# Optimization experiments

Hardware: AMD Instinct MI355X
Metric: run time of the kernel (lower is better)

Reference implementation:

```python
import jax, jax.numpy as jnp
import numpy as np

B, C_IN, H, W = 64, 2048, 14, 14
D, FF, G, NC, NH = 768, 2048, 100, 9605, 8
DF = int(NC / G + 0.999)  # 97
HD = D // NH
EPS = 1e-5


def _ln(x, g, b):
    m = jnp.mean(x, axis=-1, keepdims=True)
    v = jnp.mean(jnp.square(x - m), axis=-1, keepdims=True)
    return (x - m) * jax.lax.rsqrt(v + EPS) * g + b


def setup_inputs() -> dict:
    key = jax.random.key(0)
    ks = jax.random.split(key, 16)
    def xav(k, shape):
        fan_in, fan_out = shape[-1], shape[-2] if len(shape) > 1 else shape[-1]
        std = float(np.sqrt(2.0 / (fan_in + fan_out)))
        return jax.random.normal(k, shape, jnp.float32) * std
    return {
        "x": jax.random.normal(ks[0], (B, C_IN, H, W), jnp.float32),
        "w_embed": xav(ks[1], (D, C_IN)), "b_embed": jnp.zeros((D,), jnp.float32),
        "query_embed": jax.random.normal(ks[2], (G, D), jnp.float32),
        "wq": xav(ks[3], (D, D)), "bq": jnp.zeros((D,), jnp.float32),
        "wk": xav(ks[4], (D, D)), "bk": jnp.zeros((D,), jnp.float32),
        "wv": xav(ks[5], (D, D)), "bv": jnp.zeros((D,), jnp.float32),
        "wo": xav(ks[6], (D, D)), "bo": jnp.zeros((D,), jnp.float32),
        "g1": jnp.ones((D,), jnp.float32), "be1": jnp.zeros((D,), jnp.float32),
        "g2": jnp.ones((D,), jnp.float32), "be2": jnp.zeros((D,), jnp.float32),
        "g3": jnp.ones((D,), jnp.float32), "be3": jnp.zeros((D,), jnp.float32),
        "w1": xav(ks[7], (FF, D)), "bl1": jnp.zeros((FF,), jnp.float32),
        "w2": xav(ks[8], (D, FF)), "bl2": jnp.zeros((D,), jnp.float32),
        "dup_pool": xav(ks[9], (G, D, DF)),
        "dup_bias": jnp.zeros((NC,), jnp.float32),
    }


def reference(x, w_embed, b_embed, query_embed, wq, bq, wk, bk, wv, bv, wo, bo,
              g1, be1, g2, be2, g3, be3, w1, bl1, w2, bl2, dup_pool, dup_bias):
    bs = x.shape[0]
    # [B, C, H, W] -> [B, S, C]
    mem = x.reshape(bs, x.shape[1], -1).transpose(0, 2, 1)
    # embed_standart + relu -> [B, S, D]
    mem = jax.nn.relu(jnp.einsum('bsc,dc->bsd', mem, w_embed) + b_embed)
    # tgt = queries broadcast to batch: [B, G, D]
    tgt = jnp.broadcast_to(query_embed[None], (bs, G, D))
    # layer: tgt = norm1(tgt + dropout1(tgt)) = norm1(2*tgt)
    tgt = _ln(tgt + tgt, g1, be1)
    # cross multihead attention (q=tgt, k=v=mem)
    q = (jnp.einsum('bgd,ed->bge', tgt, wq) + bq).reshape(bs, G, NH, HD)
    k = (jnp.einsum('bsd,ed->bse', mem, wk) + bk).reshape(bs, -1, NH, HD)
    v = (jnp.einsum('bsd,ed->bse', mem, wv) + bv).reshape(bs, -1, NH, HD)
    scores = jnp.einsum('bghd,bshd->bhgs', q, k) / jnp.sqrt(jnp.float32(HD))
    attn = jax.nn.softmax(scores, axis=-1)
    ctx = jnp.einsum('bhgs,bshd->bghd', attn, v).reshape(bs, G, D)
    ctx = jnp.einsum('bgd,ed->bge', ctx, wo) + bo
    tgt = _ln(tgt + ctx, g2, be2)
    # FFN
    ff = jax.nn.relu(jnp.einsum('bgd,fd->bgf', tgt, w1) + bl1)
    ff = jnp.einsum('bgf,df->bgd', ff, w2) + bl2
    h = _ln(tgt + ff, g3, be3)  # [B, G, D]
    # grouped FC: per-group matmul fused into one batched einsum
    out_extrap = jnp.einsum('bgd,gdf->bgf', h, dup_pool)  # [B, G, DF]
    logits = out_extrap.reshape(bs, G * DF)[:, :NC] + dup_bias
    return logits
```

## Files before the change

kernel.cpp:

```cpp
#include <hip/hip_runtime.h>
#include <hip/hip_bf16.h>


#define B_    64
#define CIN_  2048
#define S_    196
#define D_    768
#define FF_   2048
#define G_    100
#define NC_   9605
#define NH_   8
#define HD_   96
#define DF_   97
#define FP_   112
#define GP_   112
#define SP_   224
#define BS_   (B_ * S_)
#define BG_   (B_ * G_)

typedef __bf16 bf16x8 __attribute__((ext_vector_type(8)));
typedef float  f32x4  __attribute__((ext_vector_type(4)));
typedef ushort us8    __attribute__((ext_vector_type(8)));

__device__ __forceinline__ float bf2f(ushort u) {
  union { unsigned int i; float f; } v; v.i = ((unsigned int)u) << 16; return v.f;
}
__device__ __forceinline__ ushort f2bf(float f) {
  __hip_bfloat16 h = __float2bfloat16(f);
  return *reinterpret_cast<ushort*>(&h);
}

__device__ __forceinline__ void gl2lds16(const ushort* g, ushort* l) {
  __builtin_amdgcn_global_load_lds((const __attribute__((address_space(1))) unsigned int*)g,
                                   (__attribute__((address_space(3))) unsigned int*)l, 16, 0, 0);
}

#define DT_BLKS 400
#define XP_BLKS 2048
#define CV_BLKS 512
#define TG_BLKS 128

struct PrepArgs {
  const float* x;   ushort* aemb;
  const float* dup; ushort* dupT;
  const float* csrc[7]; ushort* cdst[7]; int cn4[7]; int ctotal;
  const float* qe; const float* g1; const float* be1;
  float* tgt; ushort* tgtB;
};

__global__ __launch_bounds__(256) void k_prep(PrepArgs pa) {
  __shared__ __align__(16) char smem[196 * 72 * 2];
  int jid = blockIdx.x;
  const int t = threadIdx.x;

  if (jid < DT_BLKS) {
    float (*tile)[33] = (float (*)[33])smem;
    const int g = jid >> 2, dchunk = jid & 3;
    const int tx = t & 31, ty = t >> 5;
    for (int di = 0; di < 6; ++di) {
      const int d0 = dchunk * 192 + di * 32;
      for (int f0 = 0; f0 < 128; f0 += 32) {
        #pragma unroll
        for (int r = 0; r < 32; r += 8) {
          int d = d0 + ty + r, f = f0 + tx;
          tile[ty + r][tx] = (f < DF_) ? pa.dup[(size_t)g * D_ * DF_ + (size_t)d * DF_ + f] : 0.f;
        }
        __syncthreads();
        #pragma unroll
        for (int r = 0; r < 32; r += 8) {
          int f = f0 + ty + r, d = d0 + tx;
          if (f < FP_) pa.dupT[((size_t)g * FP_ + f) * D_ + d] = f2bf(tile[tx][ty + r]);
        }
        __syncthreads();
      }
    }
    return;
  }
  jid -= DT_BLKS;

  if (jid < XP_BLKS) {
    ushort* xs = (ushort*)smem;
    const int b = jid >> 5, cbase = (jid & 31) * 64;
    const float* xb = pa.x + ((size_t)b * CIN_ + cbase) * S_;
    #pragma unroll
    for (int it = 0; it < 4; ++it) {
      const int u = it * 256 + t;
      if (u < 784) {
        const int j = u >> 4, cq = u & 15;
        const int s = 4 * j;
        float4 a[4];
        #pragma unroll
        for (int r = 0; r < 4; ++r)
          a[r] = *(const float4*)(xb + (size_t)(cq * 4 + r) * S_ + s);
        #pragma unroll
        for (int r = 0; r < 4; ++r) {
          ushort4 o;
          o.x = f2bf(((const float*)&a[0])[r]);
          o.y = f2bf(((const float*)&a[1])[r]);
          o.z = f2bf(((const float*)&a[2])[r]);
          o.w = f2bf(((const float*)&a[3])[r]);
          *(ushort4*)&xs[(s + r) * 72 + cq * 4] = o;
        }
      }
    }
    __syncthreads();
    const int sl = t >> 3, oct = t & 7;
    #pragma unroll
    for (int sr = 0; sr < 7; ++sr) {
      const int s = sr * 32 + sl;
      if (s < S_) {
        us8 v = *(const us8*)&xs[s * 72 + oct * 8];
        *(us8*)&pa.aemb[((size_t)(b * S_ + s)) * CIN_ + cbase + oct * 8] = v;
      }
    }
    return;
  }
  jid -= XP_BLKS;

  if (jid < CV_BLKS) {
    int i = jid * 256 + t;
    const int stride = CV_BLKS * 256;
    for (; i < pa.ctotal; i += stride) {
      int seg = 0, off = i;
      while (off >= pa.cn4[seg]) { off -= pa.cn4[seg]; ++seg; }
      const float4* sp = (const float4*)pa.csrc[seg];
      float4 v0 = sp[2 * off], v1 = sp[2 * off + 1];
      us8 o;
      o[0] = f2bf(v0.x); o[1] = f2bf(v0.y); o[2] = f2bf(v0.z); o[3] = f2bf(v0.w);
      o[4] = f2bf(v1.x); o[5] = f2bf(v1.y); o[6] = f2bf(v1.z); o[7] = f2bf(v1.w);
      ((us8*)pa.cdst[seg])[off] = o;
    }
    return;
  }
  jid -= CV_BLKS;

  float* r1 = (float*)smem;
  float* r2 = r1 + 256;
  const int g = jid;
  if (g >= G_) {
    for (int d = t; d < D_; d += 256) pa.tgtB[(size_t)g * D_ + d] = 0;
    return;
  }
  float y[3]; float s = 0.f, sq = 0.f;
  const float* row = pa.qe + (size_t)g * D_;
  #pragma unroll
  for (int i = 0; i < 3; ++i) { float v = 2.f * row[t + i * 256]; y[i] = v; s += v; sq += v * v; }
  r1[t] = s; r2[t] = sq; __syncthreads();
  for (int o = 128; o > 0; o >>= 1) { if (t < o) { r1[t] += r1[t + o]; r2[t] += r2[t + o]; } __syncthreads(); }
  const float mean = r1[0] * (1.f / D_);
  const float var  = r2[0] * (1.f / D_) - mean * mean;
  const float w = rsqrtf(var + 1e-5f);
  #pragma unroll
  for (int i = 0; i < 3; ++i) {
    int d = t + i * 256;
    float v = (y[i] - mean) * w * pa.g1[d] + pa.be1[d];
    pa.tgt[(size_t)g * D_ + d] = v;
    pa.tgtB[(size_t)g * D_ + d] = f2bf(v);
  }
}

__device__ __forceinline__ void gemm_core(const ushort* __restrict__ A, const ushort* __restrict__ B,
    const float* __restrict__ bias, const float* __restrict__ bias2,
    float* __restrict__ Cf, ushort* __restrict__ Cb, ushort* __restrict__ Vt,
    int N, int K, int m0, int n0, int relu, ushort* As, ushort* Bs) {
  const int t = threadIdx.x;
  const int lane = t & 63, wave = t >> 6;
  const int quad = lane >> 4, lrow = lane & 15;
  const int wr = (wave >> 1) * 64, wc = (wave & 1) * 64;
  const int srow = t >> 2, scol = (t & 3) * 8;
  const ushort* ag = A + (size_t)(m0 + srow) * K + scol;
  const ushort* bg = B + (size_t)(n0 + srow) * K + scol;
  ushort* asw = As + t * 8;
  ushort* bsw = Bs + t * 8;
  f32x4 acc[4][4] = {};
  gl2lds16(ag,                  asw);
  gl2lds16(ag + (size_t)64 * K, asw + 64 * 32);
  gl2lds16(bg,                  bsw);
  gl2lds16(bg + (size_t)64 * K, bsw + 64 * 32);
  int cur = 0;
  for (int k0 = 0; k0 < K; k0 += 32) {
    if (k0 + 32 < K) {
      const int nb = (cur ^ 1) * (128 * 32);
      gl2lds16(ag + k0 + 32,                  asw + nb);
      gl2lds16(ag + k0 + 32 + (size_t)64 * K, asw + nb + 64 * 32);
      gl2lds16(bg + k0 + 32,                  bsw + nb);
      gl2lds16(bg + k0 + 32 + (size_t)64 * K, bsw + nb + 64 * 32);
      asm volatile("s_waitcnt vmcnt(4)" ::: "memory");
    } else {
      asm volatile("s_waitcnt vmcnt(0)" ::: "memory");
    }
    __builtin_amdgcn_s_barrier();
    __builtin_amdgcn_sched_barrier(0);
    const ushort* as = As + cur * (128 * 32);
    const ushort* bs = Bs + cur * (128 * 32);
    bf16x8 af[4], bfr[4];
    #pragma unroll
    for (int i = 0; i < 4; ++i) af[i] = *(const bf16x8*)&as[(wr + i * 16 + lrow) * 32 + quad * 8];
    #pragma unroll
    for (int j = 0; j < 4; ++j) bfr[j] = *(const bf16x8*)&bs[(wc + j * 16 + lrow) * 32 + quad * 8];
    __builtin_amdgcn_s_setprio(1);
    #pragma unroll
    for (int i = 0; i < 4; ++i)
      #pragma unroll
      for (int j = 0; j < 4; ++j)
        acc[i][j] = __builtin_amdgcn_mfma_f32_16x16x32_bf16(af[i], bfr[j], acc[i][j], 0, 0, 0);
    __builtin_amdgcn_s_setprio(0);
    __builtin_amdgcn_sched_barrier(0);
    __builtin_amdgcn_s_barrier();
    __builtin_amdgcn_sched_barrier(0);
    cur ^= 1;
  }
  #pragma unroll
  for (int i = 0; i < 4; ++i) {
    #pragma unroll
    for (int j = 0; j < 4; ++j) {
      const int gcol = n0 + wc + j * 16 + lrow;
      const float bv = (bias2 && gcol >= D_) ? bias2[gcol - D_] : (bias ? bias[gcol] : 0.f);
      if (Vt && gcol >= D_) {
        const int dv = gcol - D_, hh = dv / HD_, hd = dv % HD_;
        const int row0 = m0 + wr + i * 16 + quad * 4;
        const int bb = row0 / S_, ss = row0 % S_;
        ushort4 o;
        o.x = f2bf(acc[i][j][0] + bv);
        o.y = f2bf(acc[i][j][1] + bv);
        o.z = f2bf(acc[i][j][2] + bv);
        o.w = f2bf(acc[i][j][3] + bv);
        *(ushort4*)&Vt[((size_t)(bb * NH_ + hh) * HD_ + hd) * SP_ + ss] = o;
      } else {
        #pragma unroll
        for (int r = 0; r < 4; ++r) {
          const int grow = m0 + wr + i * 16 + quad * 4 + r;
          float v = acc[i][j][r] + bv;
          if (relu) v = fmaxf(v, 0.f);
          if (Cf) Cf[(size_t)grow * N + gcol] = v;
          else    Cb[(size_t)grow * N + gcol] = f2bf(v);
        }
      }
    }
  }
}

__global__ __launch_bounds__(256) void k_gemm(const ushort* __restrict__ A, const ushort* __restrict__ B,
    const float* __restrict__ bias, const float* __restrict__ bias2,
    float* __restrict__ Cf, ushort* __restrict__ Cb, ushort* __restrict__ Vt,
    int N, int K, int nbx, int nm, int relu,
    const ushort* __restrict__ A2, const ushort* __restrict__ B2,
    const float* __restrict__ bias_2, ushort* __restrict__ Cb2, int N2, int K2) {
  __shared__ ushort As[2 * 128 * 32];
  __shared__ ushort Bs[2 * 128 * 32];
  const int l = blockIdx.x;
  const int base = ((nm + 7) & ~7) * nbx;
  if (l >= base) {
    gemm_core(A2, B2, bias_2, nullptr, nullptr, Cb2, nullptr, N2, K2, 0, (l - base) * 128, 0, As, Bs);
    return;
  }
  const int mb = (l >> 3) / nbx * 8 + (l & 7);
  const int nb = (l >> 3) % nbx;
  if (mb >= nm) return;
  gemm_core(A, B, bias, bias2, Cf, Cb, Vt, N, K, mb * 128, nb * 128, relu, As, Bs);
}
static inline int swz_grid(int nm, int nbx) { return ((nm + 7) & ~7) * nbx; }

__device__ __forceinline__ void gemm_core64(const ushort* __restrict__ A, const ushort* __restrict__ B,
    const float* __restrict__ bias, ushort* __restrict__ Cb,
    int N, int K, int m0, int n0, int relu, ushort* As, ushort* Bs) {
  const int t = threadIdx.x;
  const int lane = t & 63, wave = t >> 6;
  const int quad = lane >> 4, lrow = lane & 15;
  const int wr = (wave >> 1) * 32, wc = (wave & 1) * 64;
  const int srow = t >> 2, scol = (t & 3) * 8;
  const ushort* ag = A + (size_t)(m0 + srow) * K + scol;
  const ushort* bg = B + (size_t)(n0 + srow) * K + scol;
  ushort* asw = As + t * 8;
  ushort* bsw = Bs + t * 8;
  f32x4 acc[2][4] = {};
  gl2lds16(ag,                  asw);
  gl2lds16(bg,                  bsw);
  gl2lds16(bg + (size_t)64 * K, bsw + 64 * 32);
  int cur = 0;
  for (int k0 = 0; k0 < K; k0 += 32) {
    if (k0 + 32 < K) {
      gl2lds16(ag + k0 + 32,                  asw + (cur ^ 1) * (64 * 32));
      gl2lds16(bg + k0 + 32,                  bsw + (cur ^ 1) * (128 * 32));
      gl2lds16(bg + k0 + 32 + (size_t)64 * K, bsw + (cur ^ 1) * (128 * 32) + 64 * 32);
      asm volatile("s_waitcnt vmcnt(3)" ::: "memory");
    } else {
      asm volatile("s_waitcnt vmcnt(0)" ::: "memory");
    }
    __builtin_amdgcn_s_barrier();
    __builtin_amdgcn_sched_barrier(0);
    const ushort* as = As + cur * (64 * 32);
    const ushort* bs = Bs + cur * (128 * 32);
    bf16x8 af[2], bfr[4];
    #pragma unroll
    for (int i = 0; i < 2; ++i) af[i] = *(const bf16x8*)&as[(wr + i * 16 + lrow) * 32 + quad * 8];
    #pragma unroll
    for (int j = 0; j < 4; ++j) bfr[j] = *(const bf16x8*)&bs[(wc + j * 16 + lrow) * 32 + quad * 8];
    __builtin_amdgcn_s_setprio(1);
    #pragma unroll
    for (int i = 0; i < 2; ++i)
      #pragma unroll
      for (int j = 0; j < 4; ++j)
        acc[i][j] = __builtin_amdgcn_mfma_f32_16x16x32_bf16(af[i], bfr[j], acc[i][j], 0, 0, 0);
    __builtin_amdgcn_s_setprio(0);
    __builtin_amdgcn_sched_barrier(0);
    __builtin_amdgcn_s_barrier();
    __builtin_amdgcn_sched_barrier(0);
    cur ^= 1;
  }
  #pragma unroll
  for (int i = 0; i < 2; ++i) {
    #pragma unroll
    for (int j = 0; j < 4; ++j) {
      const int gcol = n0 + wc + j * 16 + lrow;
      const float bv = bias ? bias[gcol] : 0.f;
      #pragma unroll
      for (int r = 0; r < 4; ++r) {
        const int grow = m0 + wr + i * 16 + quad * 4 + r;
        float v = acc[i][j][r] + bv;
        if (relu) v = fmaxf(v, 0.f);
        Cb[(size_t)grow * N + gcol] = f2bf(v);
      }
    }
  }
}

__global__ __launch_bounds__(256) void k_gemm64(const ushort* __restrict__ A, const ushort* __restrict__ B,
    const float* __restrict__ bias, ushort* __restrict__ Cb,
    int N, int K, int nbx, int nm, int relu,
    const ushort* __restrict__ A2, const ushort* __restrict__ B2,
    const float* __restrict__ bias_2, ushort* __restrict__ Cb2, int N2, int K2, int nbx2) {
  __shared__ ushort As[2 * 64 * 32];
  __shared__ ushort Bs[2 * 128 * 32];
  const int l = blockIdx.x;
  const int base = ((nm + 7) & ~7) * nbx;
  if (l >= base) {
    const int l2 = l - base;
    gemm_core64(A2, B2, bias_2, Cb2, N2, K2, (l2 / nbx2) * 64, (l2 % nbx2) * 128, 0, As, Bs);
    return;
  }
  const int mb = (l >> 3) / nbx * 8 + (l & 7);
  const int nb = (l >> 3) % nbx;
  if (mb >= nm) return;
  gemm_core64(A, B, bias, Cb, N, K, mb * 64, nb * 128, relu, As, Bs);
}

__global__ __launch_bounds__(256) void k_attn(const ushort* __restrict__ qB,
    const ushort* __restrict__ Kb, const ushort* __restrict__ VbT, ushort* __restrict__ ctx) {
  __shared__ ushort lds[GP_ * SP_];
  ushort* Ks = lds;
  ushort* Ps = lds;
  const int h = blockIdx.x, b = blockIdx.y, t = threadIdx.x;
  const int bh = b * NH_ + h;
  const int lane = t & 63, wave = t >> 6;
  const int quad = lane >> 4, c = lane & 15;
  for (int i = t; i < 208 * 12; i += 256) {
    int r = i / 12, col = (i % 12) * 8;
    gl2lds16(Kb + ((size_t)(b * S_ + r)) * D_ + h * HD_ + col, &Ks[i * 8]);
  }
  __syncthreads();
  const float scale = 0.1020620726f;
  f32x4 p[2][13];
  #pragma unroll
  for (int rep = 0; rep < 2; ++rep) {
    const int ii = wave + rep * 4;
    if (ii >= 7) continue;
    bf16x8 af[3];
    #pragma unroll
    for (int ks = 0; ks < 3; ++ks)
      af[ks] = *(const bf16x8*)(qB + ((size_t)(ii * 16 + c)) * D_ + h * HD_ + ks * 32 + quad * 8);
    __builtin_amdgcn_s_setprio(1);
    #pragma unroll
    for (int j = 0; j < 13; ++j) {
      f32x4 a = {};
      #pragma unroll
      for (int ks = 0; ks < 3; ++ks) {
        bf16x8 bf = *(const bf16x8*)&Ks[(j * 16 + c) * HD_ + ks * 32 + quad * 8];
        a = __builtin_amdgcn_mfma_f32_16x16x32_bf16(af[ks], bf, a, 0, 0, 0);
      }
      p[rep][j] = a;
    }
    __builtin_amdgcn_s_setprio(0);
    float m[4] = {-1e30f, -1e30f, -1e30f, -1e30f};
    #pragma unroll
    for (int j = 0; j < 13; ++j)
      #pragma unroll
      for (int r = 0; r < 4; ++r) {
        float v = p[rep][j][r] * scale;
        if (j == 12 && c >= 4) v = -1e30f;
        p[rep][j][r] = v;
        m[r] = fmaxf(m[r], v);
      }
    #pragma unroll
    for (int r = 0; r < 4; ++r) {
      m[r] = fmaxf(m[r], __shfl_xor(m[r], 1));
      m[r] = fmaxf(m[r], __shfl_xor(m[r], 2));
      m[r] = fmaxf(m[r], __shfl_xor(m[r], 4));
      m[r] = fmaxf(m[r], __shfl_xor(m[r], 8));
    }
    float lsum[4] = {0.f, 0.f, 0.f, 0.f};
    #pragma unroll
    for (int j = 0; j < 13; ++j)
      #pragma unroll
      for (int r = 0; r < 4; ++r) {
        float e = __expf(p[rep][j][r] - m[r]);
        p[rep][j][r] = e; lsum[r] += e;
      }
    #pragma unroll
    for (int r = 0; r < 4; ++r) {
      lsum[r] += __shfl_xor(lsum[r], 1);
      lsum[r] += __shfl_xor(lsum[r], 2);
      lsum[r] += __shfl_xor(lsum[r], 4);
      lsum[r] += __shfl_xor(lsum[r], 8);
      lsum[r] = 1.f / lsum[r];
    }
    #pragma unroll
    for (int j = 0; j < 13; ++j)
      #pragma unroll
      for (int r = 0; r < 4; ++r)
        p[rep][j][r] *= lsum[r];
  }
  __syncthreads();
  #pragma unroll
  for (int rep = 0; rep < 2; ++rep) {
    const int ii = wave + rep * 4;
    if (ii >= 7) continue;
    #pragma unroll
    for (int r = 0; r < 4; ++r) {
      const int g = ii * 16 + quad * 4 + r;
      #pragma unroll
      for (int j = 0; j < 13; ++j)
        Ps[g * SP_ + j * 16 + c] = f2bf(p[rep][j][r]);
      Ps[g * SP_ + 208 + c] = 0;
    }
  }
  __syncthreads();
  #pragma unroll
  for (int rep = 0; rep < 2; ++rep) {
    const int ii = wave + rep * 4;
    if (ii >= 7) continue;
    bf16x8 af[7];
    #pragma unroll
    for (int k = 0; k < 7; ++k)
      af[k] = *(const bf16x8*)&Ps[(ii * 16 + c) * SP_ + k * 32 + quad * 8];
    #pragma unroll
    for (int j = 0; j < 6; ++j) {
      f32x4 acc = {};
      __builtin_amdgcn_s_setprio(1);
      #pragma unroll
      for (int k = 0; k < 7; ++k) {
        bf16x8 bf = *(const bf16x8*)(VbT + ((size_t)bh * HD_ + j * 16 + c) * SP_ + k * 32 + quad * 8);
        acc = __builtin_amdgcn_mfma_f32_16x16x32_bf16(af[k], bf, acc, 0, 0, 0);
      }
      __builtin_amdgcn_s_setprio(0);
      #pragma unroll
      for (int r = 0; r < 4; ++r) {
        const int g = ii * 16 + quad * 4 + r;
        if (g < G_)
          ctx[((size_t)(b * G_ + g)) * D_ + h * HD_ + j * 16 + c] = f2bf(acc[r]);
      }
    }
  }
}

__global__ __launch_bounds__(256) void k_lnres(const float* __restrict__ resid, int resid_mod,
    const ushort* __restrict__ addB, const float* __restrict__ gamma, const float* __restrict__ beta,
    float* __restrict__ outf, ushort* __restrict__ outb, int transb) {
  const int row = blockIdx.x, t = threadIdx.x;
  __shared__ float r1[256], r2[256];
  const float* rrow = resid + (size_t)(resid_mod ? (row % G_) : row) * D_;
  const ushort* arow = addB + (size_t)row * D_;
  float y[3]; float s = 0.f, sq = 0.f;
  #pragma unroll
  for (int i = 0; i < 3; ++i) {
    int d = t + i * 256;
    float v = rrow[d] + bf2f(arow[d]);
    y[i] = v; s += v; sq += v * v;
  }
  r1[t] = s; r2[t] = sq; __syncthreads();
  for (int o = 128; o > 0; o >>= 1) { if (t < o) { r1[t] += r1[t + o]; r2[t] += r2[t + o]; } __syncthreads(); }
  const float mean = r1[0] * (1.f / D_);
  const float var  = r2[0] * (1.f / D_) - mean * mean;
  const float w = rsqrtf(var + 1e-5f);
  const size_t orow = transb ? ((size_t)(row % G_) * B_ + row / G_) : (size_t)row;
  #pragma unroll
  for (int i = 0; i < 3; ++i) {
    int d = t + i * 256;
    float v = (y[i] - mean) * w * gamma[d] + beta[d];
    if (outf) outf[(size_t)row * D_ + d] = v;
    if (outb) outb[orow * D_ + d] = f2bf(v);
  }
}

__global__ __launch_bounds__(256) void k_head4(const ushort* __restrict__ hT,
    const ushort* __restrict__ dupT, const float* __restrict__ dup_bias, float* __restrict__ out) {
  const int g = blockIdx.x, j = blockIdx.y, t = threadIdx.x;
  const int lane = t & 63, wave = t >> 6;
  const int quad = lane >> 4, c = lane & 15;
  const ushort* ap = hT + ((size_t)g * B_ + wave * 16 + c) * D_;
  const ushort* bp = dupT + ((size_t)g * FP_ + j * 16 + c) * D_;
  f32x4 acc = {};
  #pragma unroll 8
  for (int k0 = 0; k0 < D_; k0 += 32) {
    bf16x8 af = *(const bf16x8*)(ap + k0 + quad * 8);
    bf16x8 bf = *(const bf16x8*)(bp + k0 + quad * 8);
    acc = __builtin_amdgcn_mfma_f32_16x16x32_bf16(af, bf, acc, 0, 0, 0);
  }
  const int f = j * 16 + c;
  if (f >= DF_) return;
  const int n = g * DF_ + f;
  if (n >= NC_) return;
  const float bv = dup_bias[n];
  #pragma unroll
  for (int r = 0; r < 4; ++r) {
    const int b = wave * 16 + quad * 4 + r;
    out[(size_t)b * NC_ + n] = acc[r] + bv;
  }
}

static constexpr size_t OFF_AEMB  = 0;
static constexpr size_t OFF_VBT   = 0;
static constexpr size_t OFF_FF    = 0;
static constexpr size_t OFF_FFO   = 26214400;
static constexpr size_t OFF_WEMB  = 51380224;
static constexpr size_t OFF_MEM   = 54525952;
static constexpr size_t OFF_WK    = 73793536;
static constexpr size_t OFF_WV    = 74973184;
static constexpr size_t OFF_WO    = 76152832;
static constexpr size_t OFF_W1    = 77332480;
static constexpr size_t OFF_W2    = 80478208;
static constexpr size_t OFF_DUP   = 83623936;
static constexpr size_t OFF_KB    = 100827136;
static constexpr size_t OFF_TGT   = 139362304;
static constexpr size_t OFF_TGTB  = 139669504;
static constexpr size_t OFF_Q     = 139866112;
static constexpr size_t OFF_CTX   = 140068864;
static constexpr size_t OFF_WQ    = OFF_CTX;
static constexpr size_t OFF_CTXO  = 149899264;
static constexpr size_t OFF_TGT2F = 169560064;
static constexpr size_t OFF_TGT2B = 189220864;
static constexpr size_t OFF_HB    = 199051264;

extern "C" void kernel_launch(void* const* d_in, const int* in_sizes, int n_in,
                              void* d_out, int out_size, void* d_ws, size_t ws_size,
                              hipStream_t stream) {
  const float* x           = (const float*)d_in[0];
  const float* w_embed     = (const float*)d_in[1];
  const float* b_embed     = (const float*)d_in[2];
  const float* query_embed = (const float*)d_in[3];
  const float* wq          = (const float*)d_in[4];
  const float* bq          = (const float*)d_in[5];
  const float* wk          = (const float*)d_in[6];
  const float* bk          = (const float*)d_in[7];
  const float* wv          = (const float*)d_in[8];
  const float* bv          = (const float*)d_in[9];
  const float* wo          = (const float*)d_in[10];
  const float* bo          = (const float*)d_in[11];
  const float* g1          = (const float*)d_in[12];
  const float* be1         = (const float*)d_in[13];
  const float* g2          = (const float*)d_in[14];
  const float* be2         = (const float*)d_in[15];
  const float* g3          = (const float*)d_in[16];
  const float* be3         = (const float*)d_in[17];
  const float* w1          = (const float*)d_in[18];
  const float* bl1         = (const float*)d_in[19];
  const float* w2          = (const float*)d_in[20];
  const float* bl2         = (const float*)d_in[21];
  const float* dup_pool    = (const float*)d_in[22];
  const float* dup_bias    = (const float*)d_in[23];
  float* out = (float*)d_out;
  char* ws = (char*)d_ws;

  ushort* aemb  = (ushort*)(ws + OFF_AEMB);
  ushort* wembB = (ushort*)(ws + OFF_WEMB);
  ushort* memB  = (ushort*)(ws + OFF_MEM);
  ushort* wkvB  = (ushort*)(ws + OFF_WK);
  ushort* wkB   = (ushort*)(ws + OFF_WK);
  ushort* wvB   = (ushort*)(ws + OFF_WV);
  ushort* woB   = (ushort*)(ws + OFF_WO);
  ushort* w1B   = (ushort*)(ws + OFF_W1);
  ushort* w2B   = (ushort*)(ws + OFF_W2);
  ushort* wqB   = (ushort*)(ws + OFF_WQ);
  ushort* dupT  = (ushort*)(ws + OFF_DUP);
  ushort* Kb    = (ushort*)(ws + OFF_KB);
  float*  tgtF  = (float*)(ws + OFF_TGT);
  ushort* tgtB  = (ushort*)(ws + OFF_TGTB);
  ushort* qB    = (ushort*)(ws + OFF_Q);
  ushort* VbT   = (ushort*)(ws + OFF_VBT);
  ushort* ctxB  = (ushort*)(ws + OFF_CTX);
  ushort* ctxoB = (ushort*)(ws + OFF_CTXO);
  float*  tgt2F = (float*)(ws + OFF_TGT2F);
  ushort* tgt2B = (ushort*)(ws + OFF_TGT2B);
  ushort* ffB   = (ushort*)(ws + OFF_FF);
  ushort* ffoB  = (ushort*)(ws + OFF_FFO);
  ushort* hT    = (ushort*)(ws + OFF_HB);

  PrepArgs pa;
  pa.x = x; pa.aemb = aemb;
  pa.dup = dup_pool; pa.dupT = dupT;
  pa.csrc[0] = w_embed; pa.cdst[0] = wembB; pa.cn4[0] = D_ * CIN_ / 8;
  pa.csrc[1] = wk;      pa.cdst[1] = wkB;   pa.cn4[1] = D_ * D_ / 8;
  pa.csrc[2] = wv;      pa.cdst[2] = wvB;   pa.cn4[2] = D_ * D_ / 8;
  pa.csrc[3] = wo;      pa.cdst[3] = woB;   pa.cn4[3] = D_ * D_ / 8;
  pa.csrc[4] = w1;      pa.cdst[4] = w1B;   pa.cn4[4] = FF_ * D_ / 8;
  pa.csrc[5] = w2;      pa.cdst[5] = w2B;   pa.cn4[5] = D_ * FF_ / 8;
  pa.csrc[6] = wq;      pa.cdst[6] = wqB;   pa.cn4[6] = D_ * D_ / 8;
  pa.ctotal = pa.cn4[0] + pa.cn4[1] + pa.cn4[2] + pa.cn4[3] + pa.cn4[4] + pa.cn4[5] + pa.cn4[6];
  pa.qe = query_embed; pa.g1 = g1; pa.be1 = be1; pa.tgt = tgtF; pa.tgtB = tgtB;
  k_prep<<<DT_BLKS + XP_BLKS + CV_BLKS + TG_BLKS, 256, 0, stream>>>(pa);

  k_gemm64<<<swz_grid(196, 6) + 12, 256, 0, stream>>>(aemb, wembB, b_embed, memB,
                                                      D_, CIN_, 6, 196, 1,
                                                      tgtB, wqB, bq, qB, D_, D_, 6);

  k_gemm<<<swz_grid(98, 12), 256, 0, stream>>>(memB, wkvB, bk, bv, nullptr, Kb, VbT,
                                               D_, D_, 12, 98, 0,
                                               nullptr, nullptr, nullptr, nullptr, 0, 0);

  k_attn<<<dim3(NH_, B_), 256, 0, stream>>>(qB, Kb, VbT, ctxB);

  k_gemm64<<<swz_grid(100, 6), 256, 0, stream>>>(ctxB, woB, bo, ctxoB,
                                                 D_, D_, 6, 100, 0,
                                                 nullptr, nullptr, nullptr, nullptr, 0, 0, 1);

  k_lnres<<<BG_, 256, 0, stream>>>(tgtF, 1, ctxoB, g2, be2, tgt2F, tgt2B, 0);

  k_gemm<<<swz_grid(50, 16), 256, 0, stream>>>(tgt2B, w1B, bl1, nullptr, nullptr, ffB, nullptr,
                                               FF_, D_, 16, 50, 1,
                                               nullptr, nullptr, nullptr, nullptr, 0, 0);
  k_gemm64<<<swz_grid(100, 6), 256, 0, stream>>>(ffB, w2B, bl2, ffoB,
                                                 D_, FF_, 6, 100, 0,
                                                 nullptr, nullptr, nullptr, nullptr, 0, 0, 1);

  k_lnres<<<BG_, 256, 0, stream>>>(tgt2F, 0, ffoB, g3, be3, nullptr, hT, 1);

  k_head4<<<dim3(G_, 7), 256, 0, stream>>>(hT, dupT, dup_bias, out);
}
```

Baseline: 561.4 us.

## Move weight conversion and dup transpose into the embed GEMM launch

The prep kernel now only does the x transpose, the w_embed/wq conversion and the LN of the queries. The dup_pool transpose and the wk/wv/wo/w1/w2 conversions move into a new fused k_embed launch that also runs the embed and Q-projection GEMMs. The goal is to let the bandwidth-bound conversion work overlap the compute-bound embed GEMM instead of sitting on the critical path ahead of it. The x transpose also uses smaller 32-channel blocks, doubling the block count. The cost is a heterogeneous launch where slow transpose blocks can compete with GEMM blocks for CUs.

Result: no change. 556.6 us (-0.9%).

```diff
diff --git a/kernel.cpp b/kernel.cpp
--- a/kernel.cpp
+++ b/kernel.cpp
@@ -35,58 +35,31 @@
                                    (__attribute__((address_space(3))) unsigned int*)l, 16, 0, 0);
 }
 
-#define DT_BLKS 400
-#define XP_BLKS 2048
-#define CV_BLKS 512
-#define TG_BLKS 128
+#define XP_BLKS  4096
+#define CVP_BLKS 256
+#define TG_BLKS  128
 
 struct PrepArgs {
   const float* x;   ushort* aemb;
-  const float* dup; ushort* dupT;
-  const float* csrc[7]; ushort* cdst[7]; int cn4[7]; int ctotal;
+  const float* csrc[2]; ushort* cdst[2]; int cn4[2]; int ctotal;
   const float* qe; const float* g1; const float* be1;
   float* tgt; ushort* tgtB;
 };
 
 __global__ __launch_bounds__(256) void k_prep(PrepArgs pa) {
-  __shared__ __align__(16) char smem[196 * 72 * 2];
+  __shared__ __align__(16) char smem[196 * 40 * 2];
   int jid = blockIdx.x;
   const int t = threadIdx.x;
 
-  if (jid < DT_BLKS) {
-    float (*tile)[33] = (float (*)[33])smem;
-    const int g = jid >> 2, dchunk = jid & 3;
-    const int tx = t & 31, ty = t >> 5;
-    for (int di = 0; di < 6; ++di) {
-      const int d0 = dchunk * 192 + di * 32;
-      for (int f0 = 0; f0 < 128; f0 += 32) {
-        #pragma unroll
-        for (int r = 0; r < 32; r += 8) {
-          int d = d0 + ty + r, f = f0 + tx;
-          tile[ty + r][tx] = (f < DF_) ? pa.dup[(size_t)g * D_ * DF_ + (size_t)d * DF_ + f] : 0.f;
-        }
-        __syncthreads();
-        #pragma unroll
-        for (int r = 0; r < 32; r += 8) {
-          int f = f0 + ty + r, d = d0 + tx;
-          if (f < FP_) pa.dupT[((size_t)g * FP_ + f) * D_ + d] = f2bf(tile[tx][ty + r]);
-        }
-        __syncthreads();
-      }
-    }
-    return;
-  }
-  jid -= DT_BLKS;
-
   if (jid < XP_BLKS) {
     ushort* xs = (ushort*)smem;
-    const int b = jid >> 5, cbase = (jid & 31) * 64;
+    const int b = jid >> 6, cbase = (jid & 63) * 32;
     const float* xb = pa.x + ((size_t)b * CIN_ + cbase) * S_;
     #pragma unroll
-    for (int it = 0; it < 4; ++it) {
+    for (int it = 0; it < 2; ++it) {
       const int u = it * 256 + t;
-      if (u < 784) {
-        const int j = u >> 4, cq = u & 15;
+      if (u < 392) {
+        const int j = u >> 3, cq = u & 7;
         const int s = 4 * j;
         float4 a[4];
         #pragma unroll
@@ -99,17 +72,17 @@
           o.y = f2bf(((const float*)&a[1])[r]);
           o.z = f2bf(((const float*)&a[2])[r]);
           o.w = f2bf(((const float*)&a[3])[r]);
-          *(ushort4*)&xs[(s + r) * 72 + cq * 4] = o;
+          *(ushort4*)&xs[(s + r) * 40 + cq * 4] = o;
         }
       }
     }
     __syncthreads();
-    const int sl = t >> 3, oct = t & 7;
-    #pragma unroll
-    for (int sr = 0; sr < 7; ++sr) {
-      const int s = sr * 32 + sl;
+    const int sl = t >> 2, oct = t & 3;
+    #pragma unroll
+    for (int sr = 0; sr < 4; ++sr) {
+      const int s = sr * 64 + sl;
       if (s < S_) {
-        us8 v = *(const us8*)&xs[s * 72 + oct * 8];
+        us8 v = *(const us8*)&xs[s * 40 + oct * 8];
         *(us8*)&pa.aemb[((size_t)(b * S_ + s)) * CIN_ + cbase + oct * 8] = v;
       }
     }
@@ -117,9 +90,9 @@
   }
   jid -= XP_BLKS;
 
-  if (jid < CV_BLKS) {
+  if (jid < CVP_BLKS) {
     int i = jid * 256 + t;
-    const int stride = CV_BLKS * 256;
+    const int stride = CVP_BLKS * 256;
     for (; i < pa.ctotal; i += stride) {
       int seg = 0, off = i;
       while (off >= pa.cn4[seg]) { off -= pa.cn4[seg]; ++seg; }
@@ -132,7 +105,7 @@
     }
     return;
   }
-  jid -= CV_BLKS;
+  jid -= CVP_BLKS;
 
   float* r1 = (float*)smem;
   float* r2 = r1 + 256;
@@ -243,17 +216,10 @@
 __global__ __launch_bounds__(256) void k_gemm(const ushort* __restrict__ A, const ushort* __restrict__ B,
     const float* __restrict__ bias, const float* __restrict__ bias2,
     float* __restrict__ Cf, ushort* __restrict__ Cb, ushort* __restrict__ Vt,
-    int N, int K, int nbx, int nm, int relu,
-    const ushort* __restrict__ A2, const ushort* __restrict__ B2,
-    const float* __restrict__ bias_2, ushort* __restrict__ Cb2, int N2, int K2) {
+    int N, int K, int nbx, int nm, int relu) {
   __shared__ ushort As[2 * 128 * 32];
   __shared__ ushort Bs[2 * 128 * 32];
   const int l = blockIdx.x;
-  const int base = ((nm + 7) & ~7) * nbx;
-  if (l >= base) {
-    gemm_core(A2, B2, bias_2, nullptr, nullptr, Cb2, nullptr, N2, K2, 0, (l - base) * 128, 0, As, Bs);
-    return;
-  }
   const int mb = (l >> 3) / nbx * 8 + (l & 7);
   const int nb = (l >> 3) % nbx;
   if (mb >= nm) return;
@@ -327,22 +293,86 @@
 
 __global__ __launch_bounds__(256) void k_gemm64(const ushort* __restrict__ A, const ushort* __restrict__ B,
     const float* __restrict__ bias, ushort* __restrict__ Cb,
-    int N, int K, int nbx, int nm, int relu,
-    const ushort* __restrict__ A2, const ushort* __restrict__ B2,
-    const float* __restrict__ bias_2, ushort* __restrict__ Cb2, int N2, int K2, int nbx2) {
+    int N, int K, int nbx, int nm, int relu) {
   __shared__ ushort As[2 * 64 * 32];
   __shared__ ushort Bs[2 * 128 * 32];
   const int l = blockIdx.x;
-  const int base = ((nm + 7) & ~7) * nbx;
-  if (l >= base) {
-    const int l2 = l - base;
-    gemm_core64(A2, B2, bias_2, Cb2, N2, K2, (l2 / nbx2) * 64, (l2 % nbx2) * 128, 0, As, Bs);
-    return;
-  }
   const int mb = (l >> 3) / nbx * 8 + (l & 7);
   const int nb = (l >> 3) % nbx;
   if (mb >= nm) return;
   gemm_core64(A, B, bias, Cb, N, K, mb * 64, nb * 128, relu, As, Bs);
+}
+
+#define DT2_BLKS 400
+#define EG_BLKS  1200
+#define QP_BLKS  12
+#define CV2_BLKS 256
+
+struct EmbArgs {
+  const ushort* aemb; const ushort* wembB; const float* b_embed; ushort* memB;
+  const ushort* tgtB; const ushort* wqB;   const float* bq;      ushort* qB;
+  const float* dup; ushort* dupT;
+  const float* csrc[5]; ushort* cdst[5]; int cn4[5]; int ctotal;
+};
+
+__global__ __launch_bounds__(256) void k_embed(EmbArgs ea) {
+  __shared__ ushort As[2 * 64 * 32];
+  __shared__ ushort Bs[2 * 128 * 32];
+  int l = blockIdx.x;
+  const int t = threadIdx.x;
+
+  if (l < DT2_BLKS) {
+    float (*tile)[33] = (float (*)[33])As;
+    const int g = l >> 2, dchunk = l & 3;
+    const int tx = t & 31, ty = t >> 5;
+    for (int di = 0; di < 6; ++di) {
+      const int d0 = dchunk * 192 + di * 32;
+      for (int f0 = 0; f0 < 128; f0 += 32) {
+        #pragma unroll
+        for (int r = 0; r < 32; r += 8) {
+          int d = d0 + ty + r, f = f0 + tx;
+          tile[ty + r][tx] = (f < DF_) ? ea.dup[(size_t)g * D_ * DF_ + (size_t)d * DF_ + f] : 0.f;
+        }
+        __syncthreads();
+        #pragma unroll
+        for (int r = 0; r < 32; r += 8) {
+          int f = f0 + ty + r, d = d0 + tx;
+          if (f < FP_) ea.dupT[((size_t)g * FP_ + f) * D_ + d] = f2bf(tile[tx][ty + r]);
+        }
+        __syncthreads();
+      }
+    }
+    return;
+  }
+  l -= DT2_BLKS;
+
+  if (l < EG_BLKS) {
+    const int mb = (l >> 3) / 6 * 8 + (l & 7);
+    const int nb = (l >> 3) % 6;
+    if (mb >= 196) return;
+    gemm_core64(ea.aemb, ea.wembB, ea.b_embed, ea.memB, D_, CIN_, mb * 64, nb * 128, 1, As, Bs);
+    return;
+  }
+  l -= EG_BLKS;
+
+  if (l < QP_BLKS) {
+    gemm_core64(ea.tgtB, ea.wqB, ea.bq, ea.qB, D_, D_, (l / 6) * 64, (l % 6) * 128, 0, As, Bs);
+    return;
+  }
+  l -= QP_BLKS;
+
+  int i = l * 256 + t;
+  const int stride = CV2_BLKS * 256;
+  for (; i < ea.ctotal; i += stride) {
+    int seg = 0, off = i;
+    while (off >= ea.cn4[seg]) { off -= ea.cn4[seg]; ++seg; }
+    const float4* sp = (const float4*)ea.csrc[seg];
+    float4 v0 = sp[2 * off], v1 = sp[2 * off + 1];
+    us8 o;
+    o[0] = f2bf(v0.x); o[1] = f2bf(v0.y); o[2] = f2bf(v0.z); o[3] = f2bf(v0.w);
+    o[4] = f2bf(v1.x); o[5] = f2bf(v1.y); o[6] = f2bf(v1.z); o[7] = f2bf(v1.w);
+    ((us8*)ea.cdst[seg])[off] = o;
+  }
 }
 
 __global__ __launch_bounds__(256) void k_attn(const ushort* __restrict__ qB,
@@ -597,40 +627,36 @@
 
   PrepArgs pa;
   pa.x = x; pa.aemb = aemb;
-  pa.dup = dup_pool; pa.dupT = dupT;
   pa.csrc[0] = w_embed; pa.cdst[0] = wembB; pa.cn4[0] = D_ * CIN_ / 8;
-  pa.csrc[1] = wk;      pa.cdst[1] = wkB;   pa.cn4[1] = D_ * D_ / 8;
-  pa.csrc[2] = wv;      pa.cdst[2] = wvB;   pa.cn4[2] = D_ * D_ / 8;
-  pa.csrc[3] = wo;      pa.cdst[3] = woB;   pa.cn4[3] = D_ * D_ / 8;
-  pa.csrc[4] = w1;      pa.cdst[4] = w1B;   pa.cn4[4] = FF_ * D_ / 8;
-  pa.csrc[5] = w2;      pa.cdst[5] = w2B;   pa.cn4[5] = D_ * FF_ / 8;
-  pa.csrc[6] = wq;      pa.cdst[6] = wqB;   pa.cn4[6] = D_ * D_ / 8;
-  pa.ctotal = pa.cn4[0] + pa.cn4[1] + pa.cn4[2] + pa.cn4[3] + pa.cn4[4] + pa.cn4[5] + pa.cn4[6];
+  pa.csrc[1] = wq;      pa.cdst[1] = wqB;   pa.cn4[1] = D_ * D_ / 8;
+  pa.ctotal = pa.cn4[0] + pa.cn4[1];
   pa.qe = query_embed; pa.g1 = g1; pa.be1 = be1; pa.tgt = tgtF; pa.tgtB = tgtB;
-  k_prep<<<DT_BLKS + XP_BLKS + CV_BLKS + TG_BLKS, 256, 0, stream>>>(pa);
-
-  k_gemm64<<<swz_grid(196, 6) + 12, 256, 0, stream>>>(aemb, wembB, b_embed, memB,
-                                                      D_, CIN_, 6, 196, 1,
-                                                      tgtB, wqB, bq, qB, D_, D_, 6);
+  k_prep<<<XP_BLKS + CVP_BLKS + TG_BLKS, 256, 0, stream>>>(pa);
+
+  EmbArgs ea;
+  ea.aemb = aemb; ea.wembB = wembB; ea.b_embed = b_embed; ea.memB = memB;
+  ea.tgtB = tgtB; ea.wqB = wqB; ea.bq = bq; ea.qB = qB;
+  ea.dup = dup_pool; ea.dupT = dupT;
+  ea.csrc[0] = wk; ea.cdst[0] = wkB; ea.cn4[0] = D_ * D_ / 8;
+  ea.csrc[1] = wv; ea.cdst[1] = wvB; ea.cn4[1] = D_ * D_ / 8;
+  ea.csrc[2] = wo; ea.cdst[2] = woB; ea.cn4[2] = D_ * D_ / 8;
+  ea.csrc[3] = w1; ea.cdst[3] = w1B; ea.cn4[3] = FF_ * D_ / 8;
+  ea.csrc[4] = w2; ea.cdst[4] = w2B; ea.cn4[4] = D_ * FF_ / 8;
+  ea.ctotal = ea.cn4[0] + ea.cn4[1] + ea.cn4[2] + ea.cn4[3] + ea.cn4[4];
+  k_embed<<<DT2_BLKS + EG_BLKS + QP_BLKS + CV2_BLKS, 256, 0, stream>>>(ea);
 
   k_gemm<<<swz_grid(98, 12), 256, 0, stream>>>(memB, wkvB, bk, bv, nullptr, Kb, VbT,
-                                               D_, D_, 12, 98, 0,
-                                               nullptr, nullptr, nullptr, nullptr, 0, 0);
+                                               D_, D_, 12, 98, 0);
 
   k_attn<<<dim3(NH_, B_), 256, 0, stream>>>(qB, Kb, VbT, ctxB);
 
-  k_gemm64<<<swz_grid(100, 6), 256, 0, stream>>>(ctxB, woB, bo, ctxoB,
-                                                 D_, D_, 6, 100, 0,
-                                                 nullptr, nullptr, nullptr, nullptr, 0, 0, 1);
+  k_gemm64<<<swz_grid(100, 6), 256, 0, stream>>>(ctxB, woB, bo, ctxoB, D_, D_, 6, 100, 0);
 
   k_lnres<<<BG_, 256, 0, stream>>>(tgtF, 1, ctxoB, g2, be2, tgt2F, tgt2B, 0);
 
   k_gemm<<<swz_grid(50, 16), 256, 0, stream>>>(tgt2B, w1B, bl1, nullptr, nullptr, ffB, nullptr,
-                                               FF_, D_, 16, 50, 1,
-                                               nullptr, nullptr, nullptr, nullptr, 0, 0);
-  k_gemm64<<<swz_grid(100, 6), 256, 0, stream>>>(ffB, w2B, bl2, ffoB,
-                                                 D_, FF_, 6, 100, 0,
-                                                 nullptr, nullptr, nullptr, nullptr, 0, 0, 1);
+                                               FF_, D_, 16, 50, 1);
+  k_gemm64<<<swz_grid(100, 6), 256, 0, stream>>>(ffB, w2B, bl2, ffoB, D_, FF_, 6, 100, 0);
 
   k_lnres<<<BG_, 256, 0, stream>>>(tgt2F, 0, ffoB, g3, be3, nullptr, hT, 1);
 
```
